# Optimization experiments

Measured on AMD Instinct MI355X. Metric: run time of the kernel, lower is better.

## Reference

```python
import jax, jax.numpy as jnp
import numpy as np

N = 100_000   # nodes
E = 1_600_000 # edges (avg degree 16)
SLOPE = 0.01  # LeakyReLU default negative slope


def _lrelu(x):
    return jnp.where(x > 0, x, SLOPE * x)


def _gcn(x, W, b, src, dst, n):
    # PyG GCNConv: add self-loops, symmetric deg^{-1/2} normalization, scatter-add at dst.
    x = x @ W
    loops = jnp.arange(n)
    s = jnp.concatenate([src, loops])
    d = jnp.concatenate([dst, loops])
    deg = jax.ops.segment_sum(jnp.ones(s.shape[0], x.dtype), d, num_segments=n)
    dis = jnp.where(deg > 0, jax.lax.rsqrt(deg), 0.0)
    norm = dis[s] * dis[d]                      # [E+N]
    out = jax.ops.segment_sum(x[s] * norm[:, None], d, num_segments=n)
    return out + b


def setup_inputs() -> dict:
    key = jax.random.key(0)
    ks = jax.random.split(key, 32)
    f = lambda i, s: jax.random.normal(ks[i], s, dtype=jnp.float32) * 0.05
    inp = {
        'des': f(0, (N, 768)),
        'tweet': f(1, (N, 768)),
        'num_prop': f(2, (N, 7)),
        'cat_prop': f(3, (N, 11)),
        'new_feature': f(4, (N, 1)),
        'edge_index': jax.random.randint(ks[5], (2, E), 0, N),
        'edge_type': jax.random.randint(ks[6], (E,), 0, 2),
        # encoder linears (in,out layout; y = x @ W + b)
        'W_des': f(7, (768, 28)),  'b_des': f(8, (28,)),
        'W_tweet': f(9, (768, 36)), 'b_tweet': f(10, (36,)),
        'W_num': f(11, (7, 12)),   'b_num': f(12, (12,)),
        'W_cat': f(13, (11, 40)),  'b_cat': f(14, (40,)),
        'W_nf': f(15, (1, 12)),    'b_nf': f(16, (12,)),
        'W_in': f(17, (128, 128)), 'b_in': f(18, (128,)),
        'W_gcn1': f(19, (128, 128)), 'b_gcn1': f(20, (128,)),
        'W_gcn2': f(21, (128, 128)), 'b_gcn2': f(22, (128,)),
        'W_o1': f(23, (128, 128)), 'b_o1': f(24, (128,)),
        'W_o2': f(25, (128, 2)),   'b_o2': f(26, (2,)),
    }
    return inp


def reference(des, tweet, num_prop, cat_prop, new_feature, edge_index, edge_type,
              W_des, b_des, W_tweet, b_tweet, W_num, b_num, W_cat, b_cat,
              W_nf, b_nf, W_in, b_in, W_gcn1, b_gcn1, W_gcn2, b_gcn2,
              W_o1, b_o1, W_o2, b_o2):
    del edge_type  # accepted but unused by ESABotGCN.forward
    d = _lrelu(des @ W_des + b_des)
    t = _lrelu(tweet @ W_tweet + b_tweet)
    n = _lrelu(num_prop @ W_num + b_num)
    c = _lrelu(cat_prop @ W_cat + b_cat)
    nf = _lrelu(new_feature @ W_nf + b_nf)
    x = jnp.concatenate([d, t, n, c, nf], axis=1)   # [N,128]
    x = _lrelu(x @ W_in + b_in)
    src, dst = edge_index[0], edge_index[1]
    x = _gcn(x, W_gcn1, b_gcn1, src, dst, x.shape[0])
    # F.dropout with training=False (eval) is identity
    x = _gcn(x, W_gcn2, b_gcn2, src, dst, x.shape[0])
    x = _lrelu(x @ W_o1 + b_o1)
    return x @ W_o2 + b_o2                          # [N,2]
```

## Files before the change

### kernel.cpp

```cpp
#include <hip/hip_runtime.h>

static __device__ __forceinline__ float lrelu(float x){ return x > 0.f ? x : 0.01f*x; }

__global__ __launch_bounds__(256) void k_hist(const int* __restrict__ dst, int* __restrict__ cnt, int E){
  int e = blockIdx.x*256 + threadIdx.x;
  if (e < E) atomicAdd(&cnt[dst[e]], 1);
}

__global__ __launch_bounds__(256) void k_scan1(const int* __restrict__ cnt, int* __restrict__ rowptr,
                                               int* __restrict__ bsum, int n){
  __shared__ int sh[256];
  const int t = threadIdx.x;
  const int base = blockIdx.x*1024 + t*4;
  int v0 = (base+0<n)? cnt[base+0]:0;
  int v1 = (base+1<n)? cnt[base+1]:0;
  int v2 = (base+2<n)? cnt[base+2]:0;
  int v3 = (base+3<n)? cnt[base+3]:0;
  int s = v0+v1+v2+v3;
  sh[t] = s; __syncthreads();
  #pragma unroll
  for (int off=1; off<256; off<<=1){
    int u = (t>=off)? sh[t-off] : 0;
    __syncthreads();
    sh[t] += u;
    __syncthreads();
  }
  int ex = sh[t] - s;
  if (base+0<n) rowptr[base+0] = ex;
  if (base+1<n) rowptr[base+1] = ex+v0;
  if (base+2<n) rowptr[base+2] = ex+v0+v1;
  if (base+3<n) rowptr[base+3] = ex+v0+v1+v2;
  if (t==255) bsum[blockIdx.x] = sh[255];
}
__global__ __launch_bounds__(256) void k_scan2(int* __restrict__ bsum, int nb){
  __shared__ int sh[256];
  const int t = threadIdx.x;
  int s = (t<nb)? bsum[t] : 0;
  sh[t] = s; __syncthreads();
  #pragma unroll
  for (int off=1; off<256; off<<=1){
    int u = (t>=off)? sh[t-off] : 0;
    __syncthreads();
    sh[t] += u;
    __syncthreads();
  }
  if (t<nb) bsum[t] = sh[t] - s;
}
__global__ __launch_bounds__(256) void k_scan3(int* __restrict__ rowptr, const int* __restrict__ bsum,
                                               const int* __restrict__ cnt, float* __restrict__ dis,
                                               int* __restrict__ cursor, int n, int E){
  int i = blockIdx.x*256 + threadIdx.x;
  if (i < n){
    int r = rowptr[i] + bsum[i>>10];
    rowptr[i] = r;
    cursor[i] = r;
    dis[i] = rsqrtf((float)cnt[i] + 1.0f);
  }
  if (i==0) rowptr[n] = E;
}
__global__ __launch_bounds__(256) void k_fill(const int* __restrict__ src, const int* __restrict__ dst,
                                              int* __restrict__ cursor, int* __restrict__ csr, int E){
  int e = blockIdx.x*256 + threadIdx.x;
  if (e < E){
    int pos = atomicAdd(&cursor[dst[e]], 1);
    csr[pos] = src[e];
  }
}

__global__ __launch_bounds__(256) void k_gather(
    const float* __restrict__ yp, const int* __restrict__ rowptr,
    const int* __restrict__ csr, const float* __restrict__ dis,
    const float* __restrict__ bias, float* __restrict__ out, int n)
{
  int node = blockIdx.x*4 + (threadIdx.x>>6);
  if (node >= n) return;
  const int lane = threadIdx.x & 63;
  float2 acc = *(const float2*)(yp + (size_t)node*128 + lane*2);
  int j = rowptr[node], end = rowptr[node+1];
  for (; j+4<=end; j+=4){
    int s0=csr[j], s1=csr[j+1], s2=csr[j+2], s3=csr[j+3];
    float2 v0 = *(const float2*)(yp + (size_t)s0*128 + lane*2);
    float2 v1 = *(const float2*)(yp + (size_t)s1*128 + lane*2);
    float2 v2 = *(const float2*)(yp + (size_t)s2*128 + lane*2);
    float2 v3 = *(const float2*)(yp + (size_t)s3*128 + lane*2);
    acc.x += (v0.x+v1.x) + (v2.x+v3.x);
    acc.y += (v0.y+v1.y) + (v2.y+v3.y);
  }
  for (; j<end; ++j){
    int s = csr[j];
    float2 v = *(const float2*)(yp + (size_t)s*128 + lane*2);
    acc.x += v.x; acc.y += v.y;
  }
  float dd = dis[node];
  float2 b = *(const float2*)(bias + lane*2);
  float2 o = { acc.x*dd + b.x, acc.y*dd + b.y };
  *(float2*)(out + (size_t)node*128 + lane*2) = o;
}

template<int CP>
__device__ __forceinline__ void enc_phase768(
    const float* __restrict__ X, const float* __restrict__ W, const float* __restrict__ b,
    float (*xt)[65], float (*wt)[40], float (*xcat)[132],
    int col_off, int row0, int n, int tid)
{
  const int r = tid & 63, cg = tid >> 6;
  const int NC = CP*4;
  float acc[CP];
  #pragma unroll
  for (int j=0;j<CP;++j) acc[j]=0.f;
  for (int kt=0; kt<12; ++kt){
    __syncthreads();
    #pragma unroll
    for (int it=0; it<4; ++it){
      int f = tid + it*256;
      int rr = f >> 4, k4 = f & 15;
      float4 v = make_float4(0.f,0.f,0.f,0.f);
      if (row0 + rr < n) v = *(const float4*)(X + (size_t)(row0+rr)*768 + kt*64 + k4*4);
      xt[k4*4+0][rr]=v.x; xt[k4*4+1][rr]=v.y; xt[k4*4+2][rr]=v.z; xt[k4*4+3][rr]=v.w;
    }
    for (int idx = tid; idx < 64*NC; idx += 256){
      int k = idx / NC, j = idx % NC;
      wt[k][j] = W[(size_t)(kt*64+k)*NC + j];
    }
    __syncthreads();
    #pragma unroll 8
    for (int k=0;k<64;++k){
      float xv = xt[k][r];
      #pragma unroll
      for (int j=0;j<CP;++j) acc[j] += xv * wt[k][cg*CP + j];
    }
  }
  #pragma unroll
  for (int j=0;j<CP;++j){
    int c = cg*CP + j;
    xcat[r][col_off + c] = lrelu(acc[j] + b[c]);
  }
}

template<int K, int CP>
__device__ __forceinline__ void enc_small(
    const float* __restrict__ X, const float* __restrict__ W, const float* __restrict__ b,
    float (*xcat)[132], int col_off, int row0, int n, int tid)
{
  const int r = tid & 63, cg = tid >> 6;
  const int NC = CP*4;
  float xr[K];
  #pragma unroll
  for (int k=0;k<K;++k) xr[k] = (row0 + r < n) ? X[(size_t)(row0+r)*K + k] : 0.f;
  #pragma unroll
  for (int j=0;j<CP;++j){
    int c = cg*CP + j;
    float a = b[c];
    #pragma unroll
    for (int k=0;k<K;++k) a += xr[k]*W[k*NC + c];
    xcat[r][col_off + c] = lrelu(a);
  }
}

__global__ __launch_bounds__(256) void k_encoder(
    const float* __restrict__ des, const float* __restrict__ tweet,
    const float* __restrict__ nump, const float* __restrict__ catp,
    const float* __restrict__ nfp,
    const float* __restrict__ Wd, const float* __restrict__ bd,
    const float* __restrict__ Wt, const float* __restrict__ bt,
    const float* __restrict__ Wn, const float* __restrict__ bn,
    const float* __restrict__ Wc, const float* __restrict__ bc,
    const float* __restrict__ Wf, const float* __restrict__ bf_,
    const float* __restrict__ Wi, const float* __restrict__ bi,
    float* __restrict__ x0, int n)
{
  __shared__ float xt[64][65];
  __shared__ float wt[64][40];
  __shared__ float xcat[64][132];
  __shared__ float win[32][128];
  const int tid = threadIdx.x;
  const int row0 = blockIdx.x * 64;

  enc_phase768<7>(des,   Wd, bd, xt, wt, xcat, 0,   row0, n, tid);
  enc_phase768<9>(tweet, Wt, bt, xt, wt, xcat, 28,  row0, n, tid);
  enc_small<7,3>(nump,  Wn, bn, xcat, 64,  row0, n, tid);
  enc_small<11,10>(catp, Wc, bc, xcat, 76, row0, n, tid);
  enc_small<1,3>(nfp,   Wf, bf_, xcat, 116, row0, n, tid);

  const int tc = tid & 15, tr = tid >> 4;
  float a2[4][8];
  #pragma unroll
  for (int r=0;r<4;++r)
    #pragma unroll
    for (int c=0;c<8;++c) a2[r][c]=0.f;

  for (int kt=0; kt<4; ++kt){
    __syncthreads();
    #pragma unroll
    for (int it=0;it<4;++it){
      int f = tid + it*256;
      int rk = f >> 5, c4 = f & 31;
      *(float4*)(&win[rk][c4*4]) = *(const float4*)(Wi + (size_t)(kt*32+rk)*128 + c4*4);
    }
    __syncthreads();
    #pragma unroll 4
    for (int k=0;k<32;++k){
      float av[4];
      #pragma unroll
      for (int rr=0;rr<4;++rr) av[rr] = xcat[tr*4+rr][kt*32+k];
      float4 w0 = *(const float4*)(&win[k][tc*8]);
      float4 w1 = *(const float4*)(&win[k][tc*8+4]);
      #pragma unroll
      for (int rr=0;rr<4;++rr){
        a2[rr][0] += av[rr]*w0.x; a2[rr][1] += av[rr]*w0.y;
        a2[rr][2] += av[rr]*w0.z; a2[rr][3] += av[rr]*w0.w;
        a2[rr][4] += av[rr]*w1.x; a2[rr][5] += av[rr]*w1.y;
        a2[rr][6] += av[rr]*w1.z; a2[rr][7] += av[rr]*w1.w;
      }
    }
  }
  float4 bv0 = *(const float4*)(bi + tc*8);
  float4 bv1 = *(const float4*)(bi + tc*8 + 4);
  #pragma unroll
  for (int rr=0;rr<4;++rr){
    int row = row0 + tr*4 + rr;
    if (row < n){
      float4 o0 = { lrelu(a2[rr][0]+bv0.x), lrelu(a2[rr][1]+bv0.y),
                    lrelu(a2[rr][2]+bv0.z), lrelu(a2[rr][3]+bv0.w) };
      float4 o1 = { lrelu(a2[rr][4]+bv1.x), lrelu(a2[rr][5]+bv1.y),
                    lrelu(a2[rr][6]+bv1.z), lrelu(a2[rr][7]+bv1.w) };
      *(float4*)(x0 + (size_t)row*128 + tc*8)     = o0;
      *(float4*)(x0 + (size_t)row*128 + tc*8 + 4) = o1;
    }
  }
}

template<int ACT, int FINAL, int SCALE>
__global__ __launch_bounds__(256) void k_gemm128(
    const float* __restrict__ X, const float* __restrict__ W, const float* __restrict__ bias,
    float* __restrict__ Y, const float* __restrict__ W2, const float* __restrict__ b2,
    const float* __restrict__ scale, int n)
{
  __shared__ float xs[64][132];
  __shared__ float wt[32][128];
  const int tid = threadIdx.x;
  const int row0 = blockIdx.x * 64;

  #pragma unroll
  for (int it=0; it<8; ++it){
    int f = tid + it*256;
    int r = f >> 5, c4 = f & 31;
    float4 v = make_float4(0.f,0.f,0.f,0.f);
    if (row0 + r < n) v = *(const float4*)(X + (size_t)(row0+r)*128 + c4*4);
    *(float4*)(&xs[r][c4*4]) = v;
  }
  const int tc = tid & 15, tr = tid >> 4;
  float a2[4][8];
  #pragma unroll
  for (int r=0;r<4;++r)
    #pragma unroll
    for (int c=0;c<8;++c) a2[r][c]=0.f;

  for (int kt=0; kt<4; ++kt){
    __syncthreads();
    #pragma unroll
    for (int it=0;it<4;++it){
      int f = tid + it*256;
      int rk = f >> 5, c4 = f & 31;
      *(float4*)(&wt[rk][c4*4]) = *(const float4*)(W + (size_t)(kt*32+rk)*128 + c4*4);
    }
    __syncthreads();
    #pragma unroll 4
    for (int k=0;k<32;++k){
      float av[4];
      #pragma unroll
      for (int rr=0;rr<4;++rr) av[rr] = xs[tr*4+rr][kt*32+k];
      float4 w0 = *(const float4*)(&wt[k][tc*8]);
      float4 w1 = *(const float4*)(&wt[k][tc*8+4]);
      #pragma unroll
      for (int rr=0;rr<4;++rr){
        a2[rr][0] += av[rr]*w0.x; a2[rr][1] += av[rr]*w0.y;
        a2[rr][2] += av[rr]*w0.z; a2[rr][3] += av[rr]*w0.w;
        a2[rr][4] += av[rr]*w1.x; a2[rr][5] += av[rr]*w1.y;
        a2[rr][6] += av[rr]*w1.z; a2[rr][7] += av[rr]*w1.w;
      }
    }
  }

  float vv[4][8];
  #pragma unroll
  for (int rr=0;rr<4;++rr){
    #pragma unroll
    for (int cc=0;cc<8;++cc){
      float v = a2[rr][cc];
      if (ACT) { v += bias[tc*8+cc]; v = lrelu(v); }
      vv[rr][cc] = v;
    }
  }

  if (!FINAL){
    #pragma unroll
    for (int rr=0;rr<4;++rr){
      int row = row0 + tr*4 + rr;
      if (row < n){
        float s = SCALE ? scale[row] : 1.0f;
        float4 o0 = { vv[rr][0]*s, vv[rr][1]*s, vv[rr][2]*s, vv[rr][3]*s };
        float4 o1 = { vv[rr][4]*s, vv[rr][5]*s, vv[rr][6]*s, vv[rr][7]*s };
        *(float4*)(Y + (size_t)row*128 + tc*8)     = o0;
        *(float4*)(Y + (size_t)row*128 + tc*8 + 4) = o1;
      }
    }
  } else {
    __syncthreads();
    #pragma unroll
    for (int rr=0;rr<4;++rr)
      #pragma unroll
      for (int cc=0;cc<8;++cc) xs[tr*4+rr][tc*8+cc] = vv[rr][cc];
    __syncthreads();
    if (tid < 128){
      int r = tid & 63, j = tid >> 6;
      float a = b2[j];
      #pragma unroll 8
      for (int k=0;k<128;++k) a += xs[r][k]*W2[k*2 + j];
      int row = row0 + r;
      if (row < n) Y[(size_t)row*2 + j] = a;
    }
  }
}

extern "C" void kernel_launch(void* const* d_in, const int* in_sizes, int n_in,
                              void* d_out, int out_size, void* d_ws, size_t ws_size,
                              hipStream_t stream)
{
  (void)n_in; (void)out_size; (void)ws_size;
  const float* des   = (const float*)d_in[0];
  const float* tweet = (const float*)d_in[1];
  const float* nump  = (const float*)d_in[2];
  const float* catp  = (const float*)d_in[3];
  const float* nfp   = (const float*)d_in[4];
  const int*   eidx  = (const int*)d_in[5];
  const float* Wd = (const float*)d_in[7];  const float* bd = (const float*)d_in[8];
  const float* Wt = (const float*)d_in[9];  const float* bt = (const float*)d_in[10];
  const float* Wn = (const float*)d_in[11]; const float* bn = (const float*)d_in[12];
  const float* Wc = (const float*)d_in[13]; const float* bc = (const float*)d_in[14];
  const float* Wf = (const float*)d_in[15]; const float* bf_ = (const float*)d_in[16];
  const float* Wi = (const float*)d_in[17]; const float* bi = (const float*)d_in[18];
  const float* Wg1 = (const float*)d_in[19]; const float* bg1 = (const float*)d_in[20];
  const float* Wg2 = (const float*)d_in[21]; const float* bg2 = (const float*)d_in[22];
  const float* Wo1 = (const float*)d_in[23]; const float* bo1 = (const float*)d_in[24];
  const float* Wo2 = (const float*)d_in[25]; const float* bo2 = (const float*)d_in[26];

  const int n = in_sizes[0] / 768;
  const int E = in_sizes[5] / 2;
  const int* srcp = eidx;
  const int* dstp = eidx + E;

  float* bufA = (float*)d_ws;
  float* bufB = bufA + (size_t)n*128;
  float* dis  = bufB + (size_t)n*128;
  int*  cnt    = (int*)(dis + n);
  int*  rowptr = cnt + n;
  int*  cursor = rowptr + n + 1;
  int*  bsum   = cursor + n;
  int*  csr    = bsum + 256;

  const int gb1  = (n + 255)/256;
  const int gbe  = (E + 255)/256;
  const int grow = (n + 63)/64;
  const int nb   = (n + 1023)/1024;
  const int gag  = (n + 3)/4;

  hipMemsetAsync(cnt, 0, (size_t)n*sizeof(int), stream);
  k_hist <<<gbe, 256, 0, stream>>>(dstp, cnt, E);
  k_scan1<<<nb,  256, 0, stream>>>(cnt, rowptr, bsum, n);
  k_scan2<<<1,   256, 0, stream>>>(bsum, nb);
  k_scan3<<<gb1, 256, 0, stream>>>(rowptr, bsum, cnt, dis, cursor, n, E);
  k_fill <<<gbe, 256, 0, stream>>>(srcp, dstp, cursor, csr, E);

  k_encoder<<<grow, 256, 0, stream>>>(des,tweet,nump,catp,nfp,
      Wd,bd, Wt,bt, Wn,bn, Wc,bc, Wf,bf_, Wi,bi, bufA, n);

  k_gemm128<0,0,1><<<grow, 256, 0, stream>>>(bufA, Wg1, nullptr, bufB, nullptr, nullptr, dis, n);
  k_gather<<<gag, 256, 0, stream>>>(bufB, rowptr, csr, dis, bg1, bufA, n);

  k_gemm128<0,0,1><<<grow, 256, 0, stream>>>(bufA, Wg2, nullptr, bufB, nullptr, nullptr, dis, n);
  k_gather<<<gag, 256, 0, stream>>>(bufB, rowptr, csr, dis, bg2, bufA, n);

  k_gemm128<1,1,0><<<grow, 256, 0, stream>>>(bufA, Wo1, bo1, (float*)d_out, Wo2, bo2, nullptr, n);
}
```

Baseline: 1.913 ms.

## Split fused encoder into separate des/tweet projection kernels plus final encoder

The monolithic encoder kernel is split into two per-input 768-wide projection kernels that write into a 64-column intermediate buffer, and a final kernel that adds the small-feature encoders and the 128x128 input layer. The aim is to lower shared memory and register use per block so more blocks fit on each CU, which should improve latency hiding on the bandwidth-bound 768-wide reads. In exchange it adds two kernel launches and an extra global write and read of an N x 64 intermediate.

Result: faster. 1.854 ms (-3.1%).

```diff
diff --git a/kernel.cpp b/kernel.cpp
--- a/kernel.cpp
+++ b/kernel.cpp
@@ -6,7 +6,6 @@
   int e = blockIdx.x*256 + threadIdx.x;
   if (e < E) atomicAdd(&cnt[dst[e]], 1);
 }
-
 __global__ __launch_bounds__(256) void k_scan1(const int* __restrict__ cnt, int* __restrict__ rowptr,
                                                int* __restrict__ bsum, int n){
   __shared__ int sh[256];
@@ -98,16 +97,21 @@
 }
 
 template<int CP>
-__device__ __forceinline__ void enc_phase768(
+__global__ __launch_bounds__(256) void k_enc768(
     const float* __restrict__ X, const float* __restrict__ W, const float* __restrict__ b,
-    float (*xt)[65], float (*wt)[40], float (*xcat)[132],
-    int col_off, int row0, int n, int tid)
-{
+    float* __restrict__ xc, int col_off, int n)
+{
+  constexpr int NC = CP*4;
+  __shared__ float xt[64][65];
+  __shared__ float wt[64][NC];
+  const int tid = threadIdx.x;
   const int r = tid & 63, cg = tid >> 6;
-  const int NC = CP*4;
+  const int row0 = blockIdx.x * 64;
+
   float acc[CP];
   #pragma unroll
   for (int j=0;j<CP;++j) acc[j]=0.f;
+
   for (int kt=0; kt<12; ++kt){
     __syncthreads();
     #pragma unroll
@@ -130,17 +134,19 @@
       for (int j=0;j<CP;++j) acc[j] += xv * wt[k][cg*CP + j];
     }
   }
-  #pragma unroll
-  for (int j=0;j<CP;++j){
-    int c = cg*CP + j;
-    xcat[r][col_off + c] = lrelu(acc[j] + b[c]);
+  if (row0 + r < n){
+    #pragma unroll
+    for (int j=0;j<CP;++j){
+      int c = cg*CP + j;
+      xc[(size_t)(row0+r)*64 + col_off + c] = lrelu(acc[j] + b[c]);
+    }
   }
 }
 
 template<int K, int CP>
 __device__ __forceinline__ void enc_small(
     const float* __restrict__ X, const float* __restrict__ W, const float* __restrict__ b,
-    float (*xcat)[132], int col_off, int row0, int n, int tid)
+    float (*xs)[132], int col_off, int row0, int n, int tid)
 {
   const int r = tid & 63, cg = tid >> 6;
   const int NC = CP*4;
@@ -153,34 +159,35 @@
     float a = b[c];
     #pragma unroll
     for (int k=0;k<K;++k) a += xr[k]*W[k*NC + c];
-    xcat[r][col_off + c] = lrelu(a);
-  }
-}
-
-__global__ __launch_bounds__(256) void k_encoder(
-    const float* __restrict__ des, const float* __restrict__ tweet,
-    const float* __restrict__ nump, const float* __restrict__ catp,
-    const float* __restrict__ nfp,
-    const float* __restrict__ Wd, const float* __restrict__ bd,
-    const float* __restrict__ Wt, const float* __restrict__ bt,
+    xs[r][col_off + c] = lrelu(a);
+  }
+}
+
+__global__ __launch_bounds__(256) void k_enc_final(
+    const float* __restrict__ xc,
+    const float* __restrict__ nump, const float* __restrict__ catp, const float* __restrict__ nfp,
     const float* __restrict__ Wn, const float* __restrict__ bn,
     const float* __restrict__ Wc, const float* __restrict__ bc,
     const float* __restrict__ Wf, const float* __restrict__ bf_,
     const float* __restrict__ Wi, const float* __restrict__ bi,
     float* __restrict__ x0, int n)
 {
-  __shared__ float xt[64][65];
-  __shared__ float wt[64][40];
-  __shared__ float xcat[64][132];
+  __shared__ float xs[64][132];
   __shared__ float win[32][128];
   const int tid = threadIdx.x;
   const int row0 = blockIdx.x * 64;
 
-  enc_phase768<7>(des,   Wd, bd, xt, wt, xcat, 0,   row0, n, tid);
-  enc_phase768<9>(tweet, Wt, bt, xt, wt, xcat, 28,  row0, n, tid);
-  enc_small<7,3>(nump,  Wn, bn, xcat, 64,  row0, n, tid);
-  enc_small<11,10>(catp, Wc, bc, xcat, 76, row0, n, tid);
-  enc_small<1,3>(nfp,   Wf, bf_, xcat, 116, row0, n, tid);
+  #pragma unroll
+  for (int it=0; it<4; ++it){
+    int f = tid + it*256;
+    int r = f >> 4, c4 = f & 15;
+    float4 v = make_float4(0.f,0.f,0.f,0.f);
+    if (row0 + r < n) v = *(const float4*)(xc + (size_t)(row0+r)*64 + c4*4);
+    *(float4*)(&xs[r][c4*4]) = v;
+  }
+  enc_small<7,3>(nump,  Wn, bn, xs, 64,  row0, n, tid);
+  enc_small<11,10>(catp, Wc, bc, xs, 76, row0, n, tid);
+  enc_small<1,3>(nfp,   Wf, bf_, xs, 116, row0, n, tid);
 
   const int tc = tid & 15, tr = tid >> 4;
   float a2[4][8];
@@ -202,7 +209,7 @@
     for (int k=0;k<32;++k){
       float av[4];
       #pragma unroll
-      for (int rr=0;rr<4;++rr) av[rr] = xcat[tr*4+rr][kt*32+k];
+      for (int rr=0;rr<4;++rr) av[rr] = xs[tr*4+rr][kt*32+k];
       float4 w0 = *(const float4*)(&win[k][tc*8]);
       float4 w1 = *(const float4*)(&win[k][tc*8+4]);
       #pragma unroll
@@ -352,7 +359,8 @@
 
   float* bufA = (float*)d_ws;
   float* bufB = bufA + (size_t)n*128;
-  float* dis  = bufB + (size_t)n*128;
+  float* xc   = bufB + (size_t)n*128;
+  float* dis  = xc   + (size_t)n*64;
   int*  cnt    = (int*)(dis + n);
   int*  rowptr = cnt + n;
   int*  cursor = rowptr + n + 1;
@@ -372,8 +380,10 @@
   k_scan3<<<gb1, 256, 0, stream>>>(rowptr, bsum, cnt, dis, cursor, n, E);
   k_fill <<<gbe, 256, 0, stream>>>(srcp, dstp, cursor, csr, E);
 
-  k_encoder<<<grow, 256, 0, stream>>>(des,tweet,nump,catp,nfp,
-      Wd,bd, Wt,bt, Wn,bn, Wc,bc, Wf,bf_, Wi,bi, bufA, n);
+  k_enc768<7><<<grow, 256, 0, stream>>>(des,   Wd, bd, xc, 0,  n);
+  k_enc768<9><<<grow, 256, 0, stream>>>(tweet, Wt, bt, xc, 28, n);
+  k_enc_final<<<grow, 256, 0, stream>>>(xc, nump, catp, nfp,
+      Wn,bn, Wc,bc, Wf,bf_, Wi,bi, bufA, n);
 
   k_gemm128<0,0,1><<<grow, 256, 0, stream>>>(bufA, Wg1, nullptr, bufB, nullptr, nullptr, dis, n);
   k_gather<<<gag, 256, 0, stream>>>(bufB, rowptr, csr, dis, bg1, bufA, n);
```
